# Optimization experiments

Measured on AMD Instinct MI355X. Metric: run time of the kernel, lower is better.

The kernel has to match this reference:

```python
import jax, jax.numpy as jnp
import numpy as np
from jax import lax

DN = ('NCHW', 'OIHW', 'NCHW')

def conv7(x, w, b):
    y = lax.conv_general_dilated(x, w, window_strides=(1, 1), padding='VALID', dimension_numbers=DN)
    return y + b[None, :, None, None]

def maxpool2(x):
    return lax.reduce_window(x, -jnp.inf, lax.max, (1, 1, 2, 2), (1, 1, 2, 2), 'VALID')

def setup_inputs() -> dict:
    key = jax.random.key(0)
    ks = jax.random.split(key, 7)
    B, C, H, W = 8, 64, 70, 70
    x = jax.random.normal(ks[0], (B, C, H, W), dtype=jnp.float32)
    s = 0.05  # small init to keep softmax logits sane
    theta_w = jax.random.normal(ks[1], (100, C, 7, 7), dtype=jnp.float32) * s
    theta_b = jax.random.normal(ks[2], (100,), dtype=jnp.float32) * s
    phi_w = jax.random.normal(ks[3], (100, C, 7, 7), dtype=jnp.float32) * s
    phi_b = jax.random.normal(ks[4], (100,), dtype=jnp.float32) * s
    g_w = jax.random.normal(ks[5], (200, C, 7, 7), dtype=jnp.float32) * s
    g_b = jax.random.normal(ks[6], (200,), dtype=jnp.float32) * s
    return {'x': x, 'theta_w': theta_w, 'theta_b': theta_b, 'phi_w': phi_w, 'phi_b': phi_b, 'g_w': g_w, 'g_b': g_b}

def reference(x, theta_w, theta_b, phi_w, phi_b, g_w, g_b):
    B, C, H, W = x.shape
    h, w = H - 6, W - 6           # VALID 7x7 conv output spatial
    N = h * w                     # 4096
    M = N // 4                    # 1024 (after 2x2 maxpool)
    theta = conv7(x, theta_w, theta_b).reshape(B, 100, N)
    phi = maxpool2(conv7(x, phi_w, phi_b)).reshape(B, 100, M)
    attn = jnp.einsum('bcn,bcm->bnm', theta, phi)                # B x N x M
    attn = jax.nn.softmax(attn, axis=-1)
    g = maxpool2(conv7(x, g_w, g_b)).reshape(B, 200, M)
    attn_g = jnp.einsum('bcm,bnm->bcn', g, attn)
    return attn_g.reshape(B, 200, h, w)
```

## Files before the change

kernel.cpp:

```cpp
#include <hip/hip_runtime.h>
#include <cstdint>
#include <cstddef>

#define BATCH 8
#define CIN 64
#define HIN 70
#define HOUT 64
#define NPIX 4096
#define MPIX 1024

typedef __attribute__((ext_vector_type(8))) short short8;
typedef __attribute__((ext_vector_type(4))) float f32x4;
typedef __attribute__((ext_vector_type(4))) unsigned int uint4v;

__device__ __forceinline__ unsigned short f2bf_rne(float f) {
  unsigned int u = __builtin_bit_cast(unsigned int, f);
  unsigned int r = (u + 0x7FFFu + ((u >> 16) & 1u)) >> 16;
  return (unsigned short)r;
}

__device__ __forceinline__ unsigned int rot16(unsigned int u) {
  return (u >> 16) | (u << 16);
}

__device__ __forceinline__ short8 rot16x4(short8 v) {
  uint4v u = __builtin_bit_cast(uint4v, v);
  u.x = rot16(u.x); u.y = rot16(u.y); u.z = rot16(u.z); u.w = rot16(u.w);
  return __builtin_bit_cast(short8, u);
}

__global__ __launch_bounds__(256) void prep_all(
    const float* __restrict__ x,
    const float* __restrict__ tw, const float* __restrict__ pw,
    const float* __restrict__ gw,
    const float* __restrict__ tb, const float* __restrict__ pb,
    const float* __restrict__ gb,
    unsigned int* __restrict__ xTi, unsigned int* __restrict__ xTi_h,
    unsigned int* __restrict__ wTi, unsigned int* __restrict__ wTi_s,
    float* __restrict__ biasPad) {
  const int t = threadIdx.x;
  if (blockIdx.x < 560) {
    __shared__ float tile[64][71];
    const int blk = blockIdx.x;
    const int b = blk / 70;
    const int r = blk - b * 70;
    for (int i = t; i < 64 * 70; i += 256) {
      int ci = i / 70;
      int c = i - ci * 70;
      tile[ci][c] = x[(((size_t)(b * 64 + ci)) * 70 + r) * 70 + c];
    }
    __syncthreads();
    for (int i = t; i < 70 * 64; i += 256) {
      int c = i >> 6;
      int ci = i & 63;
      float a = tile[ci][c];
      unsigned short hi = f2bf_rne(a);
      float hif = __builtin_bit_cast(float, ((unsigned int)hi) << 16);
      unsigned short lo = f2bf_rne(a - hif);
      xTi[(((size_t)(b * 70 + r)) * 70 + c) * 64 + ci] =
          (unsigned int)hi | (((unsigned int)lo) << 16);
    }
    for (int i = t; i < 70 * 32; i += 256) {
      int c = i >> 5;
      int dwi = i & 31;
      unsigned int h0 = f2bf_rne(tile[2 * dwi][c]);
      unsigned int h1 = f2bf_rne(tile[2 * dwi + 1][c]);
      xTi_h[(((size_t)(b * 70 + r)) * 70 + c) * 32 + dwi] = h0 | (h1 << 16);
    }
    return;
  }
  int gid = (blockIdx.x - 560) * 256 + t;
  if (gid < 1404928) {
    if (gid < 448) {
      float bv = 0.0f;
      if (gid < 100) bv = tb[gid];
      else if (gid < 200) bv = pb[gid - 100];
      else if (gid < 400) bv = gb[gid - 200];
      biasPad[gid] = bv;
    }
    int ci = gid & 63;
    int OC = (gid >> 6) % 448;
    int s = gid / (448 * 64);
    float v = 0.0f;
    if (OC < 100) v = tw[((size_t)(OC * 64 + ci)) * 49 + s];
    else if (OC < 200) v = pw[((size_t)((OC - 100) * 64 + ci)) * 49 + s];
    else if (OC < 400) v = gw[((size_t)((OC - 200) * 64 + ci)) * 49 + s];
    unsigned short hi = f2bf_rne(v);
    float hif = __builtin_bit_cast(float, ((unsigned int)hi) << 16);
    unsigned short lo = f2bf_rne(v - hif);
    wTi[gid] = (unsigned int)hi | (((unsigned int)lo) << 16);
  } else if (gid < 1404928 + 301056) {
    int g2 = gid - 1404928;
    int dwi = g2 & 31;
    int OCl = (g2 >> 5) % 192;
    int s = g2 / (192 * 32);
    int gc = 56 + OCl;
    float v0 = 0.0f, v1 = 0.0f;
    if (gc < 200) {
      v0 = gw[((size_t)(gc * 64 + 2 * dwi)) * 49 + s];
      v1 = gw[((size_t)(gc * 64 + 2 * dwi + 1)) * 49 + s];
    }
    wTi_s[g2] = (unsigned int)f2bf_rne(v0) |
                (((unsigned int)f2bf_rne(v1)) << 16);
  }
}

template <bool DUAL>
__device__ __forceinline__ void conv_body(
    char* smem, int ocy,
    const unsigned short* __restrict__ xT,
    const unsigned short* __restrict__ wT,
    const float* __restrict__ biasPad,
    unsigned int* __restrict__ thd_dw,
    unsigned int* __restrict__ phd_dw,
    unsigned short* __restrict__ gP) {
  const int LDSW = 62720;
  const int NCH = DUAL ? 4 : 2;
  const int XS = DUAL ? 128 : 64;
  const int WOCS = DUAL ? 128 : 64;
  const int WSTRIDE = DUAL ? 57344 : 12288;

  const int gx = blockIdx.x;
  const int b = gx >> 3;
  const int ptile = gx & 7;
  const int oy0 = ptile * 8;
  const int oc0 = (DUAL ? 0 : 256) + (ocy << 6);
  const int oc0W = DUAL ? oc0 : (ocy << 6);

  const int t = threadIdx.x;
  const int wv = t >> 6;
  const int l = t & 63;
  const int lm = l & 15;
  const int lg = l >> 4;

  int wdstOff_[2];
  const unsigned short* wsrc_[2];
  const int keyA = ((lm >> 1) & 3) << 4;
  const int laneA = (lm << 6) + ((lg << 4) ^ keyA);

  f32x4 acc[4][2][4];
#pragma unroll
  for (int j = 0; j < 4; ++j)
#pragma unroll
    for (int rr = 0; rr < 2; ++rr)
#pragma unroll
      for (int f = 0; f < 4; ++f) acc[j][rr][f] = (f32x4)0.0f;

  for (int chunk = 0; chunk < NCH; ++chunk) {
    for (int i = t; i < 3920; i += 256) {
      int idx70 = i >> 2;
      int s16 = i & 3;
      int rr = idx70 / 70;
      int cc = idx70 - rr * 70;
      const unsigned short* src =
          xT + ((size_t)((b * 70 + oy0 + rr) * 70 + cc)) * XS +
          (chunk << 5) + (s16 << 3);
      short8 v = *(const short8*)src;
      int dst = (idx70 << 6) + ((s16 << 4) ^ (((cc >> 1) & 3) << 4));
      *(short8*)(smem + dst) = v;
    }
    short8 wreg[2];
#pragma unroll
    for (int u2 = 0; u2 < 2; ++u2) {
      int u = t + (u2 << 8);
      int sub = u >> 8;
      int oc_t = (u >> 2) & 63;
      int q = u & 3;
      wdstOff_[u2] =
          sub * 4096 + (oc_t << 6) + ((q << 4) ^ (((oc_t >> 1) & 3) << 4));
      wsrc_[u2] = wT + (size_t)(oc0W + oc_t) * WOCS + (chunk << 5) + (q << 3);
      wreg[u2] = *(const short8*)(wsrc_[u2] + (size_t)sub * WSTRIDE);
      *(short8*)(smem + LDSW + wdstOff_[u2]) = wreg[u2];
      wreg[u2] = *(const short8*)(wsrc_[u2] + (size_t)(2 + sub) * WSTRIDE);
    }
    __syncthreads();

    for (int p = 0; p < 25; ++p) {
      const char* slotBase = smem + LDSW + ((p & 1) << 13);
#pragma unroll
      for (int halfs = 0; halfs < 2; ++halfs) {
        const int s = 2 * p + halfs;
        if (s <= 48) {
          const int ky = s / 7;
          const int kx = s - ky * 7;
          const char* wb = slotBase + (halfs << 12) + laneA;
          short8 aW[4], aS[4];
#pragma unroll
          for (int j = 0; j < 4; ++j) {
            aW[j] = *(const short8*)(wb + j * 1024);
            if (DUAL) aS[j] = rot16x4(aW[j]);
          }
          const int klx = kx + lm;
          const int key = ((klx >> 1) & 3) << 4;
#pragma unroll
          for (int rr = 0; rr < 2; ++rr) {
            const char* bbase =
                smem + ((2 * wv + rr + ky) * 70 + klx) * 64 + ((lg << 4) ^ key);
#pragma unroll
            for (int f = 0; f < 4; ++f) {
              short8 bf = *(const short8*)(bbase + f * 1024);
#pragma unroll
              for (int j = 0; j < 4; ++j) {
                acc[j][rr][f] = __builtin_amdgcn_mfma_f32_16x16x32_bf16(
                    aW[j], bf, acc[j][rr][f], 0, 0, 0);
                if (DUAL)
                  acc[j][rr][f] = __builtin_amdgcn_mfma_f32_16x16x32_bf16(
                      aS[j], bf, acc[j][rr][f], 0, 0, 0);
              }
            }
          }
        }
      }
      if (p < 24) {
#pragma unroll
        for (int u2 = 0; u2 < 2; ++u2) {
          *(short8*)(smem + LDSW + (((p + 1) & 1) << 13) + wdstOff_[u2]) =
              wreg[u2];
          if (p < 23) {
            int sub = (t + (u2 << 8)) >> 8;
            int snext = 2 * (p + 2) + sub;
            if (snext > 48) snext = 48;
            wreg[u2] = *(const short8*)(wsrc_[u2] + (size_t)snext * WSTRIDE);
          }
        }
      }
      __syncthreads();
    }
  }

  float bia[4][4];
#pragma unroll
  for (int j = 0; j < 4; ++j)
#pragma unroll
    for (int r = 0; r < 4; ++r) bia[j][r] = biasPad[oc0 + j * 16 + lg * 4 + r];

  if (DUAL) {
#pragma unroll
    for (int j = 0; j < 4; ++j) {
#pragma unroll
      for (int rr = 0; rr < 2; ++rr) {
#pragma unroll
        for (int f = 0; f < 4; ++f) {
#pragma unroll
          for (int r = 0; r < 4; ++r) {
            int ch = oc0 + j * 16 + lg * 4 + r;
            if (ch < 128) {
              int n = (oy0 + 2 * wv + rr) * 64 + f * 16 + lm;
              unsigned int outw = 0u;
              if (ch < 100) {
                float v = acc[j][rr][f][r] + bia[j][r];
                unsigned short hi = f2bf_rne(v);
                float hif =
                    __builtin_bit_cast(float, ((unsigned int)hi) << 16);
                unsigned short lo = f2bf_rne(v - hif);
                outw = (unsigned int)hi | (((unsigned int)lo) << 16);
              }
              thd_dw[(((size_t)(b << 12) + n) << 7) + ch] = outw;
            }
          }
        }
      }
    }
  }

#pragma unroll
  for (int j = 0; j < 4; ++j) {
#pragma unroll
    for (int f = 0; f < 4; ++f) {
#pragma unroll
      for (int r = 0; r < 4; ++r) {
        float v0 = acc[j][0][f][r] + bia[j][r];
        float v1 = acc[j][1][f][r] + bia[j][r];
        float vr = fmaxf(v0, v1);
        float vn = fmaxf(vr, __shfl_xor(vr, 1));
        if (!(lm & 1)) {
          int ch = oc0 + j * 16 + lg * 4 + r;
          int m = (((oy0 >> 1) + wv) << 5) + f * 8 + (lm >> 1);
          if (DUAL) {
            if (ch >= 100 && ch < 200) {
              int c = ch - 100;
              unsigned short hi = f2bf_rne(vn);
              float hif = __builtin_bit_cast(float, ((unsigned int)hi) << 16);
              unsigned short lo = f2bf_rne(vn - hif);
              phd_dw[(((size_t)(b << 10) + m) << 7) + c] =
                  (unsigned int)hi | (((unsigned int)lo) << 16);
            } else if (ch >= 200) {
              gP[((size_t)(b * 208 + (ch - 200)) << 10) + m] = f2bf_rne(vn);
              if (ch < 228)
                phd_dw[(((size_t)(b << 10) + m) << 7) + (ch - 100)] = 0u;
            }
          } else {
            int cg = ch - 200;
            if (cg < 208)
              gP[((size_t)(b * 208 + cg) << 10) + m] = f2bf_rne(vn);
          }
        }
      }
    }
  }
}

__global__ __launch_bounds__(256, 2) void convmfma_kernel(
    const unsigned short* __restrict__ xTi,
    const unsigned short* __restrict__ wTi,
    const unsigned short* __restrict__ xTi_h,
    const unsigned short* __restrict__ wTi_s,
    const float* __restrict__ biasPad,
    unsigned int* __restrict__ thd_dw,
    unsigned int* __restrict__ phd_dw,
    unsigned short* __restrict__ gP) {
  __shared__ __align__(16) char smem[62720 + 16384];
  if (blockIdx.y < 4)
    conv_body<true>(smem, blockIdx.y, xTi, wTi, biasPad, thd_dw, phd_dw, gP);
  else
    conv_body<false>(smem, blockIdx.y - 4, xTi_h, wTi_s, biasPad, thd_dw,
                     phd_dw, gP);
}

__global__ __launch_bounds__(256) void attn_kernel(
    const unsigned short* __restrict__ thd,
    const unsigned short* __restrict__ phd,
    const unsigned short* __restrict__ gP,
    float* __restrict__ out) {
  __shared__ __align__(16) float outAcc[16][212];
  __shared__ float corrL[16][33];
  __shared__ float statsL[4][16][2];
  __shared__ float mFinL[16];
  __shared__ float invL[16];

  const int bid = blockIdx.x;
  const int b = bid & 7;
  const int n0 = (bid >> 3) << 4;
  const int t = threadIdx.x;
  const int w = t >> 6;
  const int l = t & 63;
  const int lm = l & 15;
  const int lg = l >> 4;

  short8 aA[8], aS[8];
  {
    const unsigned short* ap =
        thd + (((size_t)(b << 12) + n0 + lm) << 8) + lg * 8;
#pragma unroll
    for (int kf = 0; kf < 8; ++kf) {
      short8 v = *(const short8*)(ap + kf * 32);
      aA[kf] = v;
      aS[kf] = rot16x4(v);
    }
  }

  float mRun = -3.0e38f, sRun = 0.0f;
  unsigned int Pr[8][4];

  const int src1 = ((lg & 1) << 5) + lm;
  const int src2 = src1 + 16;
  const bool hi2 = (lg >> 1) != 0;

#pragma unroll
  for (int step = 0; step < 8; ++step) {
    const int m0 = (w << 8) + (step << 5);
    f32x4 ac0 = (f32x4)0.f, ac1 = (f32x4)0.f;
    f32x4 ac0b = (f32x4)0.f, ac1b = (f32x4)0.f;
    const unsigned short* bp0 =
        phd + (((size_t)(b << 10) + m0 + lm) << 8) + lg * 8;
    const unsigned short* bp1 = bp0 + (16 << 8);
    __builtin_amdgcn_s_setprio(1);
#pragma unroll
    for (int kf = 0; kf < 4; ++kf) {
      short8 av0 = *(const short8*)(bp0 + kf * 32);
      short8 av1 = *(const short8*)(bp1 + kf * 32);
      short8 av0b = *(const short8*)(bp0 + (kf + 4) * 32);
      short8 av1b = *(const short8*)(bp1 + (kf + 4) * 32);
      ac0 = __builtin_amdgcn_mfma_f32_16x16x32_bf16(av0, aA[kf], ac0, 0, 0, 0);
      ac1 = __builtin_amdgcn_mfma_f32_16x16x32_bf16(av1, aA[kf], ac1, 0, 0, 0);
      ac0b = __builtin_amdgcn_mfma_f32_16x16x32_bf16(av0b, aA[kf + 4], ac0b, 0, 0, 0);
      ac1b = __builtin_amdgcn_mfma_f32_16x16x32_bf16(av1b, aA[kf + 4], ac1b, 0, 0, 0);
      ac0 = __builtin_amdgcn_mfma_f32_16x16x32_bf16(av0, aS[kf], ac0, 0, 0, 0);
      ac1 = __builtin_amdgcn_mfma_f32_16x16x32_bf16(av1, aS[kf], ac1, 0, 0, 0);
      ac0b = __builtin_amdgcn_mfma_f32_16x16x32_bf16(av0b, aS[kf + 4], ac0b, 0, 0, 0);
      ac1b = __builtin_amdgcn_mfma_f32_16x16x32_bf16(av1b, aS[kf + 4], ac1b, 0, 0, 0);
    }
    __builtin_amdgcn_s_setprio(0);
    ac0 += ac0b;
    ac1 += ac1b;
    float tm = fmaxf(fmaxf(fmaxf(ac0[0], ac0[1]), fmaxf(ac0[2], ac0[3])),
                     fmaxf(fmaxf(ac1[0], ac1[1]), fmaxf(ac1[2], ac1[3])));
    tm = fmaxf(tm, __shfl_xor(tm, 16));
    tm = fmaxf(tm, __shfl_xor(tm, 32));
    float mNew = fmaxf(mRun, tm);
    float scale = __expf(mRun - mNew);
    float p0 = __expf(ac0[0] - mNew), p1 = __expf(ac0[1] - mNew);
    float p2 = __expf(ac0[2] - mNew), p3 = __expf(ac0[3] - mNew);
    float q0 = __expf(ac1[0] - mNew), q1 = __expf(ac1[1] - mNew);
    float q2 = __expf(ac1[2] - mNew), q3 = __expf(ac1[3] - mNew);
    float cs = ((p0 + p1) + (p2 + p3)) + ((q0 + q1) + (q2 + q3));
    cs += __shfl_xor(cs, 16);
    cs += __shfl_xor(cs, 32);
    mRun = mNew;
    sRun = sRun * scale + cs;
    if (l < 16) corrL[lm][(w << 3) + step] = mRun;
    unsigned int d0 = (unsigned int)f2bf_rne(p0) |
                      (((unsigned int)f2bf_rne(p1)) << 16);
    unsigned int d1 = (unsigned int)f2bf_rne(p2) |
                      (((unsigned int)f2bf_rne(p3)) << 16);
    unsigned int e0 = (unsigned int)f2bf_rne(q0) |
                      (((unsigned int)f2bf_rne(q1)) << 16);
    unsigned int e1 = (unsigned int)f2bf_rne(q2) |
                      (((unsigned int)f2bf_rne(q3)) << 16);
    unsigned int A0 = (unsigned int)__shfl((int)d0, src1);
    unsigned int A1 = (unsigned int)__shfl((int)d1, src1);
    unsigned int B0 = (unsigned int)__shfl((int)d0, src2);
    unsigned int B1 = (unsigned int)__shfl((int)d1, src2);
    unsigned int C0 = (unsigned int)__shfl((int)e0, src1);
    unsigned int C1 = (unsigned int)__shfl((int)e1, src1);
    unsigned int D0 = (unsigned int)__shfl((int)e0, src2);
    unsigned int D1 = (unsigned int)__shfl((int)e1, src2);
    Pr[step][0] = hi2 ? C0 : A0;
    Pr[step][1] = hi2 ? C1 : A1;
    Pr[step][2] = hi2 ? D0 : B0;
    Pr[step][3] = hi2 ? D1 : B1;
  }
  if (l < 16) {
    statsL[w][lm][0] = mRun;
    statsL[w][lm][1] = sRun;
  }
  __syncthreads();

  if (t < 16) {
    float mF = -3.0e38f;
#pragma unroll
    for (int qq = 0; qq < 4; ++qq) mF = fmaxf(mF, statsL[qq][t][0]);
    float sF = 0.0f;
#pragma unroll
    for (int qq = 0; qq < 4; ++qq)
      sF += statsL[qq][t][1] * __expf(statsL[qq][t][0] - mF);
    mFinL[t] = mF;
    invL[t] = 1.0f / sF;
  }
  __syncthreads();

  {
    int e = t * 2;
#pragma unroll
    for (int i = 0; i < 2; ++i) {
      int row = (e + i) >> 5;
      int col = (e + i) & 31;
      corrL[row][col] = __expf(corrL[row][col] - mFinL[row]) * invL[row];
    }
  }
  __syncthreads();

#pragma unroll
  for (int s = 0; s < 8; ++s) {
    float corr = corrL[lm][(w << 3) + s];
#pragma unroll
    for (int j = 0; j < 4; ++j) {
      unsigned int u = Pr[s][j];
      float lo = __builtin_bit_cast(float, u << 16);
      float hi = __builtin_bit_cast(float, u & 0xffff0000u);
      Pr[s][j] = (unsigned int)f2bf_rne(lo * corr) |
                 (((unsigned int)f2bf_rne(hi * corr)) << 16);
    }
  }

  f32x4 oacc[13];
#pragma unroll
  for (int i = 0; i < 13; ++i) oacc[i] = (f32x4)0.f;

  __builtin_amdgcn_s_setprio(1);
#pragma unroll
  for (int s = 0; s < 8; ++s) {
    uint4v pu;
    pu.x = Pr[s][0]; pu.y = Pr[s][1]; pu.z = Pr[s][2]; pu.w = Pr[s][3];
    short8 pf = __builtin_bit_cast(short8, pu);
    const unsigned short* gbase =
        gP + ((size_t)(b * 208) << 10) + (w << 8) + (s << 5) + lg * 8;
#pragma unroll
    for (int ct = 0; ct < 13; ++ct) {
      int c = (ct << 4) + lm;
      short8 gv = *(const short8*)(gbase + ((size_t)c << 10));
      oacc[ct] = __builtin_amdgcn_mfma_f32_16x16x32_bf16(pf, gv, oacc[ct], 0, 0, 0);
    }
  }
  __builtin_amdgcn_s_setprio(0);

  for (int rnd = 0; rnd < 4; ++rnd) {
    if (w == rnd) {
#pragma unroll
      for (int ct = 0; ct < 13; ++ct) {
#pragma unroll
        for (int r = 0; r < 4; ++r) {
          int n = (lg << 2) + r;
          int c = (ct << 4) + lm;
          if (rnd == 0) outAcc[n][c] = oacc[ct][r];
          else outAcc[n][c] += oacc[ct][r];
        }
      }
    }
    __syncthreads();
  }

  {
    int lane16 = t & 15;
    int grp = t >> 4;
    for (int c = grp; c < 200; c += 16)
      out[(((size_t)(b * 200 + c)) << 12) + n0 + lane16] = outAcc[lane16][c];
  }
}

extern "C" void kernel_launch(void* const* d_in, const int* in_sizes, int n_in,
                              void* d_out, int out_size, void* d_ws,
                              size_t ws_size, hipStream_t stream) {
  const float* x  = (const float*)d_in[0];
  const float* tw = (const float*)d_in[1];
  const float* tb = (const float*)d_in[2];
  const float* pw = (const float*)d_in[3];
  const float* pb = (const float*)d_in[4];
  const float* gw = (const float*)d_in[5];
  const float* gb = (const float*)d_in[6];
  float* out = (float*)d_out;

  unsigned short* ws_us = (unsigned short*)d_ws;
  unsigned short* thd   = ws_us;
  unsigned short* phd   = ws_us + 8388608;
  unsigned short* gP    = ws_us + 10485760;
  unsigned short* xTi   = ws_us + 12189696;
  unsigned short* wTi   = ws_us + 17207296;
  unsigned short* xTi_h = ws_us + 20017152;
  unsigned short* wTi_s = ws_us + 22525952;
  float* biasPad = (float*)(ws_us + 23128064);

  prep_all<<<560 + 6664, 256, 0, stream>>>(
      x, tw, pw, gw, tb, pb, gb, (unsigned int*)xTi, (unsigned int*)xTi_h,
      (unsigned int*)wTi, (unsigned int*)wTi_s, biasPad);

  convmfma_kernel<<<dim3(64, 7), 256, 0, stream>>>(
      xTi, wTi, xTi_h, wTi_s, biasPad, (unsigned int*)thd,
      (unsigned int*)phd, gP);
  attn_kernel<<<2048, 256, 0, stream>>>(thd, phd, gP, out);
}
```

Baseline: 408.4 us.

## Loop weight prep over kernel taps per thread; merge split MFMA accumulator chains

The weight-prep portion of prep_all now has each thread handle one (output channel, input channel) pair and loop over the 49 kernel taps, instead of one thread per element. This cuts the prep grid from 6664 weight blocks to 136 and reads each filter's 49 contiguous floats sequentially rather than with a stride-49 gather. In the attention kernel, the two independent accumulator chains used for the QK MFMAs are merged into one 8-step chain. That removes a vector add and some registers but lengthens the dependent MFMA chain. The dual bf16 encoding is also factored into a helper.

```diff
diff --git a/kernel.cpp b/kernel.cpp
--- a/kernel.cpp
+++ b/kernel.cpp
@@ -27,6 +27,13 @@
   uint4v u = __builtin_bit_cast(uint4v, v);
   u.x = rot16(u.x); u.y = rot16(u.y); u.z = rot16(u.z); u.w = rot16(u.w);
   return __builtin_bit_cast(short8, u);
+}
+
+__device__ __forceinline__ unsigned int dual_enc(float v) {
+  unsigned short hi = f2bf_rne(v);
+  float hif = __builtin_bit_cast(float, ((unsigned int)hi) << 16);
+  unsigned short lo = f2bf_rne(v - hif);
+  return (unsigned int)hi | (((unsigned int)lo) << 16);
 }
 
 __global__ __launch_bounds__(256) void prep_all(
@@ -53,12 +60,7 @@
     for (int i = t; i < 70 * 64; i += 256) {
       int c = i >> 6;
       int ci = i & 63;
-      float a = tile[ci][c];
-      unsigned short hi = f2bf_rne(a);
-      float hif = __builtin_bit_cast(float, ((unsigned int)hi) << 16);
-      unsigned short lo = f2bf_rne(a - hif);
-      xTi[(((size_t)(b * 70 + r)) * 70 + c) * 64 + ci] =
-          (unsigned int)hi | (((unsigned int)lo) << 16);
+      xTi[(((size_t)(b * 70 + r)) * 70 + c) * 64 + ci] = dual_enc(tile[ci][c]);
     }
     for (int i = t; i < 70 * 32; i += 256) {
       int c = i >> 5;
@@ -70,38 +72,36 @@
     return;
   }
   int gid = (blockIdx.x - 560) * 256 + t;
-  if (gid < 1404928) {
-    if (gid < 448) {
+  if (gid < 28672) {
+    int ci = gid & 63;
+    int OC = gid >> 6;
+    const float* srcp = nullptr;
+    if (OC < 100) srcp = tw + (size_t)(OC * 64 + ci) * 49;
+    else if (OC < 200) srcp = pw + (size_t)((OC - 100) * 64 + ci) * 49;
+    else if (OC < 400) srcp = gw + (size_t)((OC - 200) * 64 + ci) * 49;
+    if (ci == 0) {
       float bv = 0.0f;
-      if (gid < 100) bv = tb[gid];
-      else if (gid < 200) bv = pb[gid - 100];
-      else if (gid < 400) bv = gb[gid - 200];
-      biasPad[gid] = bv;
-    }
-    int ci = gid & 63;
-    int OC = (gid >> 6) % 448;
-    int s = gid / (448 * 64);
-    float v = 0.0f;
-    if (OC < 100) v = tw[((size_t)(OC * 64 + ci)) * 49 + s];
-    else if (OC < 200) v = pw[((size_t)((OC - 100) * 64 + ci)) * 49 + s];
-    else if (OC < 400) v = gw[((size_t)((OC - 200) * 64 + ci)) * 49 + s];
-    unsigned short hi = f2bf_rne(v);
-    float hif = __builtin_bit_cast(float, ((unsigned int)hi) << 16);
-    unsigned short lo = f2bf_rne(v - hif);
-    wTi[gid] = (unsigned int)hi | (((unsigned int)lo) << 16);
-  } else if (gid < 1404928 + 301056) {
-    int g2 = gid - 1404928;
+      if (OC < 100) bv = tb[OC];
+      else if (OC < 200) bv = pb[OC - 100];
+      else if (OC < 400) bv = gb[OC - 200];
+      biasPad[OC] = bv;
+    }
+    for (int s = 0; s < 49; ++s) {
+      float v = srcp ? srcp[s] : 0.0f;
+      wTi[((size_t)s * 448 + OC) * 64 + ci] = dual_enc(v);
+    }
+  } else if (gid < 28672 + 6144) {
+    int g2 = gid - 28672;
     int dwi = g2 & 31;
-    int OCl = (g2 >> 5) % 192;
-    int s = g2 / (192 * 32);
+    int OCl = g2 >> 5;
     int gc = 56 + OCl;
-    float v0 = 0.0f, v1 = 0.0f;
-    if (gc < 200) {
-      v0 = gw[((size_t)(gc * 64 + 2 * dwi)) * 49 + s];
-      v1 = gw[((size_t)(gc * 64 + 2 * dwi + 1)) * 49 + s];
-    }
-    wTi_s[g2] = (unsigned int)f2bf_rne(v0) |
-                (((unsigned int)f2bf_rne(v1)) << 16);
+    const float* s0 = (gc < 200) ? gw + (size_t)(gc * 64 + 2 * dwi) * 49 : nullptr;
+    const float* s1 = (gc < 200) ? gw + (size_t)(gc * 64 + 2 * dwi + 1) * 49 : nullptr;
+    for (int s = 0; s < 49; ++s) {
+      unsigned int h0 = s0 ? (unsigned int)f2bf_rne(s0[s]) : 0u;
+      unsigned int h1 = s1 ? (unsigned int)f2bf_rne(s1[s]) : 0u;
+      wTi_s[((size_t)s * 192 + OCl) * 32 + dwi] = h0 | (h1 << 16);
+    }
   }
 }
 
@@ -247,14 +247,7 @@
             if (ch < 128) {
               int n = (oy0 + 2 * wv + rr) * 64 + f * 16 + lm;
               unsigned int outw = 0u;
-              if (ch < 100) {
-                float v = acc[j][rr][f][r] + bia[j][r];
-                unsigned short hi = f2bf_rne(v);
-                float hif =
-                    __builtin_bit_cast(float, ((unsigned int)hi) << 16);
-                unsigned short lo = f2bf_rne(v - hif);
-                outw = (unsigned int)hi | (((unsigned int)lo) << 16);
-              }
+              if (ch < 100) outw = dual_enc(acc[j][rr][f][r] + bia[j][r]);
               thd_dw[(((size_t)(b << 12) + n) << 7) + ch] = outw;
             }
           }
@@ -278,12 +271,7 @@
           int m = (((oy0 >> 1) + wv) << 5) + f * 8 + (lm >> 1);
           if (DUAL) {
             if (ch >= 100 && ch < 200) {
-              int c = ch - 100;
-              unsigned short hi = f2bf_rne(vn);
-              float hif = __builtin_bit_cast(float, ((unsigned int)hi) << 16);
-              unsigned short lo = f2bf_rne(vn - hif);
-              phd_dw[(((size_t)(b << 10) + m) << 7) + c] =
-                  (unsigned int)hi | (((unsigned int)lo) << 16);
+              phd_dw[(((size_t)(b << 10) + m) << 7) + (ch - 100)] = dual_enc(vn);
             } else if (ch >= 200) {
               gP[((size_t)(b * 208 + (ch - 200)) << 10) + m] = f2bf_rne(vn);
               if (ch < 228)
@@ -360,29 +348,20 @@
   for (int step = 0; step < 8; ++step) {
     const int m0 = (w << 8) + (step << 5);
     f32x4 ac0 = (f32x4)0.f, ac1 = (f32x4)0.f;
-    f32x4 ac0b = (f32x4)0.f, ac1b = (f32x4)0.f;
     const unsigned short* bp0 =
         phd + (((size_t)(b << 10) + m0 + lm) << 8) + lg * 8;
     const unsigned short* bp1 = bp0 + (16 << 8);
     __builtin_amdgcn_s_setprio(1);
 #pragma unroll
-    for (int kf = 0; kf < 4; ++kf) {
+    for (int kf = 0; kf < 8; ++kf) {
       short8 av0 = *(const short8*)(bp0 + kf * 32);
       short8 av1 = *(const short8*)(bp1 + kf * 32);
-      short8 av0b = *(const short8*)(bp0 + (kf + 4) * 32);
-      short8 av1b = *(const short8*)(bp1 + (kf + 4) * 32);
       ac0 = __builtin_amdgcn_mfma_f32_16x16x32_bf16(av0, aA[kf], ac0, 0, 0, 0);
       ac1 = __builtin_amdgcn_mfma_f32_16x16x32_bf16(av1, aA[kf], ac1, 0, 0, 0);
-      ac0b = __builtin_amdgcn_mfma_f32_16x16x32_bf16(av0b, aA[kf + 4], ac0b, 0, 0, 0);
-      ac1b = __builtin_amdgcn_mfma_f32_16x16x32_bf16(av1b, aA[kf + 4], ac1b, 0, 0, 0);
       ac0 = __builtin_amdgcn_mfma_f32_16x16x32_bf16(av0, aS[kf], ac0, 0, 0, 0);
       ac1 = __builtin_amdgcn_mfma_f32_16x16x32_bf16(av1, aS[kf], ac1, 0, 0, 0);
-      ac0b = __builtin_amdgcn_mfma_f32_16x16x32_bf16(av0b, aS[kf + 4], ac0b, 0, 0, 0);
-      ac1b = __builtin_amdgcn_mfma_f32_16x16x32_bf16(av1b, aS[kf + 4], ac1b, 0, 0, 0);
     }
     __builtin_amdgcn_s_setprio(0);
-    ac0 += ac0b;
-    ac1 += ac1b;
     float tm = fmaxf(fmaxf(fmaxf(ac0[0], ac0[1]), fmaxf(ac0[2], ac0[3])),
                      fmaxf(fmaxf(ac1[0], ac1[1]), fmaxf(ac1[2], ac1[3])));
     tm = fmaxf(tm, __shfl_xor(tm, 16));
@@ -530,7 +509,7 @@
   unsigned short* wTi_s = ws_us + 22525952;
   float* biasPad = (float*)(ws_us + 23128064);
 
-  prep_all<<<560 + 6664, 256, 0, stream>>>(
+  prep_all<<<560 + 136, 256, 0, stream>>>(
       x, tw, pw, gw, tb, pb, gb, (unsigned int*)xTi, (unsigned int*)xTi_h,
       (unsigned int*)wTi, (unsigned int*)wTi_s, biasPad);
 
```

After: 419.7 us. 1.03x slower.
